# Optimization experiments

Measured on AMD Instinct MI355X. Metric: run time of the kernel, lower is better.

## Reference

```python
import jax, jax.numpy as jnp
import numpy as np

NP_, NB_, E_, BE_ = 10000, 30000, 300000, 8192
PIN, BIN, EA = 128, 128, 16
HID, GH = 64, 4
D, TH, L, NC, SEQ = 128, 4, 2, 10, 6


def _ln(x, g, b, eps=1e-5):
    m = x.mean(-1, keepdims=True)
    v = ((x - m) ** 2).mean(-1, keepdims=True)
    return (x - m) * jax.lax.rsqrt(v + eps) * g + b


def _seg_softmax(e, seg, n):
    m = jax.ops.segment_max(e, seg, num_segments=n)
    m = jnp.where(jnp.isfinite(m), m, 0.0)
    ex = jnp.exp(e - m[seg])
    s = jax.ops.segment_sum(ex, seg, num_segments=n)
    return ex / (s[seg] + 1e-16)


def _gatv2(xs, xd, es, ed, ea, Wl, bl, Wr, br, We, att, bias, n_dst):
    # PyG GATv2Conv, concat=False, add_self_loops=False, eval mode (no dropout)
    xl = (xs @ Wl + bl).reshape(-1, GH, HID)   # [Ns,H,C] source transform (message content)
    xr = (xd @ Wr + br).reshape(-1, GH, HID)   # [Nd,H,C] dest transform
    eh = (ea @ We).reshape(-1, GH, HID)        # [E,H,C] edge transform (no bias in PyG)
    msg = xl[es] + xr[ed] + eh                 # [E,H,C]
    score = jnp.einsum('ehc,hc->eh', jax.nn.leaky_relu(msg, 0.2), att)
    alpha = _seg_softmax(score, ed, n_dst)     # softmax over in-edges per dest node
    out = jax.ops.segment_sum(alpha[..., None] * xl[es], ed, num_segments=n_dst)
    return out.mean(axis=1) + bias             # concat=False -> mean over heads


def _mha(x, Wqkv, bqkv, Wo, bo):
    S, d = x.shape
    dh = d // TH
    q, k, v = jnp.split(x @ Wqkv + bqkv, 3, axis=-1)
    q = q.reshape(S, TH, dh).transpose(1, 0, 2)
    k = k.reshape(S, TH, dh).transpose(1, 0, 2)
    v = v.reshape(S, TH, dh).transpose(1, 0, 2)
    a = jax.nn.softmax(jnp.einsum('hqd,hkd->hqk', q, k) / jnp.sqrt(jnp.float32(dh)), axis=-1)
    o = jnp.einsum('hqk,hkd->hqd', a, v).transpose(1, 0, 2).reshape(S, d)
    return o @ Wo + bo


def _forward(pitcher_feat, batter_feat, edge_attr, history_states,
             Wp, bp, Wb, bb,
             rel_Wl, rel_bl, rel_Wr, rel_br, rel_We, rel_att, rel_bias,
             rev_Wl, rev_bl, rev_Wr, rev_br, rev_We, rev_att, rev_bias,
             Wgs, bgs, Wet, bet, pos,
             Wqkv, bqkv, Wo, bo, ln1g, ln1b, W1, b1, W2, b2, ln2g, ln2b,
             Wc1, bc1, Wc2, bc2,
             edge_src, edge_dst, edge_ids):
    gelu = lambda t: jax.nn.gelu(t, approximate=False)
    px = gelu(pitcher_feat @ Wp + bp)
    bx = gelu(batter_feat @ Wb + bb)
    # ('pitcher','faces','batter'): messages pitcher->batter, aggregated at batter nodes
    h_b = gelu(_gatv2(px, bx, edge_src, edge_dst, edge_attr,
                      rel_Wl, rel_bl, rel_Wr, rel_br, rel_We, rel_att, rel_bias, bx.shape[0]))
    # reversed relation: batter->pitcher, aggregated at pitcher nodes
    h_p = gelu(_gatv2(bx, px, edge_dst, edge_src, edge_attr,
                      rev_Wl, rev_bl, rev_Wr, rev_br, rev_We, rev_att, rev_bias, px.shape[0]))
    state = jnp.concatenate([h_p.mean(0), h_b.mean(0), edge_attr.mean(0)], -1) @ Wgs + bgs
    tok = jnp.concatenate([h_p[edge_src[edge_ids]], h_b[edge_dst[edge_ids]],
                           edge_attr[edge_ids]], -1) @ Wet + bet
    x = jnp.concatenate([history_states, state[None]], 0) + pos[:SEQ]
    for i in range(L):  # post-LN TransformerEncoderLayer, gelu activation, eval (no dropout)
        x = _ln(x + _mha(x, Wqkv[i], bqkv[i], Wo[i], bo[i]), ln1g[i], ln1b[i])
        f = gelu(x @ W1[i] + b1[i]) @ W2[i] + b2[i]
        x = _ln(x + f, ln2g[i], ln2b[i])
    ctx = x[-1]
    cat = jnp.concatenate([tok, jnp.broadcast_to(ctx, (tok.shape[0], D))], -1)
    return gelu(cat @ Wc1 + bc1) @ Wc2 + bc2


def setup_inputs() -> dict:
    key = jax.random.key(0)
    ks = iter(jax.random.split(key, 64))
    nrm = lambda shape, s: jax.random.normal(next(ks), shape, dtype=jnp.float32) * s
    d = {
        'pitcher_feat': nrm((NP_, PIN), 1.0),
        'batter_feat': nrm((NB_, BIN), 1.0),
        'edge_attr': nrm((E_, EA), 1.0),
        'history_states': nrm((SEQ - 1, D), 1.0),
        'Wp': nrm((PIN, HID), 0.05), 'bp': jnp.zeros((HID,), jnp.float32),
        'Wb': nrm((BIN, HID), 0.05), 'bb': jnp.zeros((HID,), jnp.float32),
    }
    for p in ('rel', 'rev'):
        d[p + '_Wl'] = nrm((HID, GH * HID), 0.05)
        d[p + '_bl'] = jnp.zeros((GH * HID,), jnp.float32)
        d[p + '_Wr'] = nrm((HID, GH * HID), 0.05)
        d[p + '_br'] = jnp.zeros((GH * HID,), jnp.float32)
        d[p + '_We'] = nrm((EA, GH * HID), 0.05)
        d[p + '_att'] = nrm((GH, HID), 0.05)
        d[p + '_bias'] = jnp.zeros((HID,), jnp.float32)
    cin = 2 * HID + EA
    d['Wgs'] = nrm((cin, D), 0.05); d['bgs'] = jnp.zeros((D,), jnp.float32)
    d['Wet'] = nrm((cin, D), 0.05); d['bet'] = jnp.zeros((D,), jnp.float32)
    d['pos'] = nrm((SEQ, D), 0.02)
    d['Wqkv'] = nrm((L, D, 3 * D), 0.05); d['bqkv'] = jnp.zeros((L, 3 * D), jnp.float32)
    d['Wo'] = nrm((L, D, D), 0.05); d['bo'] = jnp.zeros((L, D), jnp.float32)
    d['ln1g'] = jnp.ones((L, D), jnp.float32); d['ln1b'] = jnp.zeros((L, D), jnp.float32)
    d['W1'] = nrm((L, D, 4 * D), 0.05); d['b1'] = jnp.zeros((L, 4 * D), jnp.float32)
    d['W2'] = nrm((L, 4 * D, D), 0.05); d['b2'] = jnp.zeros((L, D), jnp.float32)
    d['ln2g'] = jnp.ones((L, D), jnp.float32); d['ln2b'] = jnp.zeros((L, D), jnp.float32)
    d['Wc1'] = nrm((2 * D, D), 0.05); d['bc1'] = jnp.zeros((D,), jnp.float32)
    d['Wc2'] = nrm((D, NC), 0.05); d['bc2'] = jnp.zeros((NC,), jnp.float32)
    d['edge_src'] = jax.random.randint(next(ks), (E_,), 0, NP_)
    d['edge_dst'] = jax.random.randint(next(ks), (E_,), 0, NB_)
    d['edge_ids'] = jax.random.randint(next(ks), (BE_,), 0, E_)
    return d


def reference(pitcher_feat, batter_feat, edge_attr, history_states,
              Wp, bp, Wb, bb,
              rel_Wl, rel_bl, rel_Wr, rel_br, rel_We, rel_att, rel_bias,
              rev_Wl, rev_bl, rev_Wr, rev_br, rev_We, rev_att, rev_bias,
              Wgs, bgs, Wet, bet, pos,
              Wqkv, bqkv, Wo, bo, ln1g, ln1b, W1, b1, W2, b2, ln2g, ln2b,
              Wc1, bc1, Wc2, bc2,
              edge_src, edge_dst, edge_ids):
    return _forward(pitcher_feat, batter_feat, edge_attr, history_states,
                    Wp, bp, Wb, bb,
                    rel_Wl, rel_bl, rel_Wr, rel_br, rel_We, rel_att, rel_bias,
                    rev_Wl, rev_bl, rev_Wr, rev_br, rev_We, rev_att, rev_bias,
                    Wgs, bgs, Wet, bet, pos,
                    Wqkv, bqkv, Wo, bo, ln1g, ln1b, W1, b1, W2, b2, ln2g, ln2b,
                    Wc1, bc1, Wc2, bc2,
                    edge_src, edge_dst, edge_ids)
```

## Files before the change

kernel.cpp:

```cpp
#include <hip/hip_runtime.h>
#include <math.h>

#define NP 10000
#define NB 30000
#define NEDGE 300000
#define BEDGE 8192
#define EAD 16
#define HID 64
#define GH 4
#define CW 256
#define DD 128
#define SEQ 6
#define NCLS 10
#define L 2

__device__ __forceinline__ float geluf(float x){
  return 0.5f * x * (1.0f + erff(x * 0.7071067811865475f));
}

__device__ __forceinline__ float b2f(unsigned short u){
  unsigned v = ((unsigned)u) << 16;
  return __int_as_float(v);
}
__device__ __forceinline__ unsigned short f2b(float f){
  unsigned x = __float_as_uint(f);
  unsigned r = x + 0x7FFF + ((x >> 16) & 1);
  return (unsigned short)(r >> 16);
}

typedef __attribute__((ext_vector_type(8))) short bf16x8;
typedef __attribute__((ext_vector_type(4))) float f32x4;

template<int KQ, int NTILES, bool A_F32, bool GELU>
__device__ __forceinline__
void mfma_gemm_body(int bid, const void* __restrict__ Av, const float* __restrict__ W,
                    const float* __restrict__ bias, unsigned short* __restrict__ out,
                    int M, unsigned short* __restrict__ sWt)
{
  constexpr int N  = NTILES * 16;
  constexpr int KP = KQ + 8;
  int t = threadIdx.x, w = t >> 6, l = t & 63;
  int c = l & 15, g = l >> 4;
  for (int idx = t; idx < KQ*N; idx += 256){
    int k = idx / N, n = idx - k*N;
    sWt[n*KP + k] = f2b(W[idx]);
  }
  __syncthreads();
  int rowbase = bid*64 + w*16;
  int arow = rowbase + c; if (arow > M-1) arow = M-1;
  f32x4 acc[NTILES] = {};
  #pragma unroll
  for (int ks = 0; ks < KQ/32; ++ks){
    int koff = ks*32 + g*8;
    bf16x8 a;
    if constexpr (A_F32){
      const float* Af = (const float*)Av + (size_t)arow*KQ + koff;
      float4 f0 = *(const float4*)Af;
      float4 f1 = *(const float4*)(Af + 4);
      a[0]=(short)f2b(f0.x); a[1]=(short)f2b(f0.y); a[2]=(short)f2b(f0.z); a[3]=(short)f2b(f0.w);
      a[4]=(short)f2b(f1.x); a[5]=(short)f2b(f1.y); a[6]=(short)f2b(f1.z); a[7]=(short)f2b(f1.w);
    } else {
      a = *(const bf16x8*)((const unsigned short*)Av + (size_t)arow*KQ + koff);
    }
    #pragma unroll
    for (int nt = 0; nt < NTILES; ++nt){
      bf16x8 b = *(const bf16x8*)&sWt[(nt*16 + c)*KP + koff];
      acc[nt] = __builtin_amdgcn_mfma_f32_16x16x32_bf16(a, b, acc[nt], 0, 0, 0);
    }
  }
  #pragma unroll
  for (int nt = 0; nt < NTILES; ++nt){
    #pragma unroll
    for (int j = 0; j < 4; ++j){
      int row = rowbase + g*4 + j;
      if (row < M){
        int col = nt*16 + c;
        float v = acc[nt][j] + bias[col];
        if (GELU) v = geluf(v);
        out[(size_t)row*N + col] = f2b(v);
      }
    }
  }
}

__global__ __launch_bounds__(256)
void k1_count_enc(const int* __restrict__ edst, const int* __restrict__ esrc,
                  int* __restrict__ degA, int* __restrict__ degB,
                  const float* __restrict__ pit, const float* __restrict__ Wp,
                  const float* __restrict__ bp, unsigned short* __restrict__ px,
                  const float* __restrict__ bat, const float* __restrict__ Wb,
                  const float* __restrict__ bb, unsigned short* __restrict__ bx,
                  int nbCount, int nbP)
{
  __shared__ unsigned short sWt[64*136];
  int b = blockIdx.x;
  if (b < nbCount){
    int i = b*256 + threadIdx.x;
// ... 15 lines not shown
  int t = threadIdx.x, w = t >> 6, l = t & 63;
  if (t == 0) sbase = 0;
  __syncthreads();
  for (int base = 0; base < n; base += 4096){
    int i = base + t*4;
    int4 v = make_int4(0,0,0,0);
    if (i < n) v = *(const int4*)(deg + i);
    int tsum = v.x + v.y + v.z + v.w;
    int x = tsum;
    #pragma unroll
    for (int off = 1; off < 64; off <<= 1){
      int y = __shfl_up(x, off);
      if (l >= off) x += y;
    }
    if (l == 63) wsum[w] = x;
    __syncthreads();
    int woff = 0, tot = 0;
    #pragma unroll
    for (int ww = 0; ww < 16; ++ww){
      int wv = wsum[ww];
      if (ww < w) woff += wv;
      tot += wv;
    }
    int excl = sbase + woff + x - tsum;
    if (i < n){
      int e1 = excl + v.x, e2 = excl + v.x + v.y, e3 = excl + v.x + v.y + v.z;
      row_start[i]   = excl; cursor[i]   = excl;
      row_start[i+1] = e1;   cursor[i+1] = e1;
      row_start[i+2] = e2;   cursor[i+2] = e2;
      row_start[i+3] = e3;   cursor[i+3] = e3;
    }
    __syncthreads();
    if (t == 0) sbase += tot;
    __syncthreads();
  }
  if (t == 0) row_start[n] = sbase;
}

__global__ __launch_bounds__(1024)
void scan2_kernel(const int* __restrict__ degA, int* __restrict__ rsA, int* __restrict__ curA, int nA,
                  const int* __restrict__ degB, int* __restrict__ rsB, int* __restrict__ curB, int nB,
                  float* __restrict__ mvec){
  if (blockIdx.x == 0){
    scan_dev(degA, rsA, curA, nA);
  } else {
    if (threadIdx.x < 144) mvec[threadIdx.x] = 0.f;
    scan_dev(degB, rsB, curB, nB);
  }
}

__global__ __launch_bounds__(256)
void k2_scatter_proj(const int* __restrict__ edst, const int* __restrict__ esrc,
                     int* __restrict__ curA, int* __restrict__ curB,
                     int2* __restrict__ csrA, int2* __restrict__ csrB,
                     const unsigned short* __restrict__ px, const unsigned short* __restrict__ bx,
                     const float* __restrict__ rel_Wl, const float* __restrict__ rel_bl,
                     const float* __restrict__ rel_Wr, const float* __restrict__ rel_br,
                     const float* __restrict__ rev_Wl, const float* __restrict__ rev_bl,
                     const float* __restrict__ rev_Wr, const float* __restrict__ rev_br,
                     unsigned short* __restrict__ xlA, unsigned short* __restrict__ xrA,
                     unsigned short* __restrict__ xlB, unsigned short* __restrict__ xrB,
                     int nbScat, int nbP, int nbB)
{
  __shared__ unsigned short sWt[256*72];
  int b = blockIdx.x;
  if (b < nbScat){
    int i = b*256 + threadIdx.x;
    if (i < NEDGE){
      int d = edst[i], s = esrc[i];
      int p = atomicAdd(&curA[d], 1);
      csrA[p] = make_int2(i, s);
      int q = atomicAdd(&curB[s], 1);
      csrB[q] = make_int2(i, d);
    }
  } else {
    b -= nbScat;
    if (b < nbP)               mfma_gemm_body<64,16,false,false>(b,            px, rel_Wl, rel_bl, xlA, NP, sWt);
    else if (b < nbP + nbB)    mfma_gemm_body<64,16,false,false>(b-nbP,        bx, rel_Wr, rel_br, xrA, NB, sWt);
    else if (b < nbP + 2*nbB)  mfma_gemm_body<64,16,false,false>(b-nbP-nbB,    bx, rev_Wl, rev_bl, xlB, NB, sWt);
    else                       mfma_gemm_body<64,16,false,false>(b-nbP-2*nbB,  px, rev_Wr, rev_br, xrB, NP, sWt);
  }
}

#define GAT_PAIR(X0, X1, EV0, EV1, V1OK, P0MASK)                             \
  {                                                                          \
    float x0 = b2f(X0.x), x1 = b2f(X0.y), x2 = b2f(X0.z), x3 = b2f(X0.w);    \
    float y0 = b2f(X1.x), y1 = b2f(X1.y), y2 = b2f(X1.z), y3 = b2f(X1.w);    \
    float h00 = x0 + r0, h01 = x1 + r1, h02 = x2 + r2, h03 = x3 + r3;        \
    float h10 = y0 + r0, h11 = y1 + r1, h12 = y2 + r2, h13 = y3 + r3;        \
    int ia0 = __float_as_int(EV0);                                           \
    int ia1 = __float_as_int(EV1);                                           \
    _Pragma("unroll")                                                        \
    for (int k = 0; k < EAD; ++k){                                           \
      float c0 = __int_as_float(__builtin_amdgcn_readlane(ia0, k));          \
      float c1 = __int_as_float(__builtin_amdgcn_readlane(ia1, k));          \
      float4 wv = *(const float4*)&sWe[k*CW + 4*l];                          \
      h00 = fmaf(c0, wv.x, h00); h01 = fmaf(c0, wv.y, h01);                  \
      h02 = fmaf(c0, wv.z, h02); h03 = fmaf(c0, wv.w, h03);                  \
      h10 = fmaf(c1, wv.x, h10); h11 = fmaf(c1, wv.y, h11);                  \
      h12 = fmaf(c1, wv.z, h12); h13 = fmaf(c1, wv.w, h13);                  \
    }                                                                        \
    h00 = (h00 > 0.f ? h00 : 0.2f*h00) * at.x;                               \
    h01 = (h01 > 0.f ? h01 : 0.2f*h01) * at.y;                               \
    h02 = (h02 > 0.f ? h02 : 0.2f*h02) * at.z;                               \
    h03 = (h03 > 0.f ? h03 : 0.2f*h03) * at.w;                               \
    h10 = (h10 > 0.f ? h10 : 0.2f*h10) * at.x;                               \
    h11 = (h11 > 0.f ? h11 : 0.2f*h11) * at.y;                               \
    h12 = (h12 > 0.f ? h12 : 0.2f*h12) * at.z;                               \
    h13 = (h13 > 0.f ? h13 : 0.2f*h13) * at.w;                               \
    float g0 = (h00 + h01) + (h02 + h03);                                    \
    float g1 = (h10 + h11) + (h12 + h13);                                    \
    _Pragma("unroll")                                                        \
    for (int off = 1; off < 16; off <<= 1){                                  \
      g0 += __shfl_xor(g0, off);                                             \
      g1 += __shfl_xor(g1, off);                                             \
    }                                                                        \
    float gm = (V1OK) ? fmaxf(g0, g1) : g0;                                  \
    float mn = fmaxf(m, gm);                                                 \
    float cc = __expf(m - mn);                                               \
    float p0 = __expf(g0 - mn);                                              \
    if (!(P0MASK)) p0 = 0.f;                                                 \
    float p1 = (V1OK) ? __expf(g1 - mn) : 0.f;                               \
    s  = fmaf(s, cc, p0 + p1);                                               \
    a0 = fmaf(a0, cc, fmaf(p1, y0, p0*x0));                                  \
    a1 = fmaf(a1, cc, fmaf(p1, y1, p0*x1));                                  \
    a2 = fmaf(a2, cc, fmaf(p1, y2, p0*x2));                                  \
    a3 = fmaf(a3, cc, fmaf(p1, y3, p0*x3));                                  \
    m = mn;                                                                  \
  }

__global__ __launch_bounds__(256)
void gat2_kernel(const unsigned short* __restrict__ xlA_, const unsigned short* __restrict__ xrA_,
                 const float* __restrict__ WeA, const float* __restrict__ attA,
                 const float* __restrict__ biasA, const int2* __restrict__ csrA_,
                 const int* __restrict__ rsA_, float* __restrict__ houtA,
                 const unsigned short* __restrict__ xlB_, const unsigned short* __restrict__ xrB_,
                 const float* __restrict__ WeB, const float* __restrict__ attB,
                 const float* __restrict__ biasB, const int2* __restrict__ csrB_,
                 const int* __restrict__ rsB_, float* __restrict__ houtB,
                 const float* __restrict__ ea, int gsplit)
{
  __shared__ float sWe[16*CW];
  bool isA = (int)blockIdx.x < gsplit;
  const unsigned short* xl = isA ? xlA_ : xlB_;
  const unsigned short* xr = isA ? xrA_ : xrB_;
  const float* We   = isA ? WeA   : WeB;
  const float* att  = isA ? attA  : attB;
  const float* bias = isA ? biasA : biasB;
  const int2* csr   = isA ? csrA_ : csrB_;
  const int* row_start = isA ? rsA_ : rsB_;
  float* hout = isA ? houtA : houtB;
  int ndst = isA ? NB : NP;
  int bid  = isA ? (int)blockIdx.x : (int)blockIdx.x - gsplit;
  int nblk = isA ? gsplit : (int)gridDim.x - gsplit;

  int t = threadIdx.x, l = t & 63;
  for (int i = t*4; i < 16*CW; i += 1024)
    *(float4*)&sWe[i] = *(const float4*)&We[i];
  __syncthreads();
  float4 at = *(const float4*)&att[4*l];
  float4 bi = *(const float4*)&bias[(l & 15)*4];
  int wid = bid*4 + (t >> 6);
  int nw = nblk*4;
  for (int d = wid; d < ndst; d += nw){
    ushort4 ru = *(const ushort4*)(xr + (size_t)d*CW + 4*l);
    float r0 = b2f(ru.x), r1 = b2f(ru.y), r2 = b2f(ru.z), r3 = b2f(ru.w);
    int rs = row_start[d], re = row_start[d+1];
    float m = -INFINITY, s = 0.f;
    float a0 = 0.f, a1 = 0.f, a2 = 0.f, a3 = 0.f;
    if (rs < re){
      int last = re - 1;
      #define CLMP(x) ((x) > last ? last : (x))
      int2 qA0 = csr[rs],         qA1 = csr[CLMP(rs+1)];
      int2 qB0 = csr[CLMP(rs+2)], qB1 = csr[CLMP(rs+3)];
      int2 nA0 = csr[CLMP(rs+4)], nA1 = csr[CLMP(rs+5)];
      int2 nB0 = csr[CLMP(rs+6)], nB1 = csr[CLMP(rs+7)];
      ushort4 xA0 = *(const ushort4*)(xl + (size_t)qA0.y*CW + 4*l);
      ushort4 xA1 = *(const ushort4*)(xl + (size_t)qA1.y*CW + 4*l);
      float  evA0 = ea[(size_t)qA0.x*EAD + (l & 15)];
      float  evA1 = ea[(size_t)qA1.x*EAD + (l & 15)];
      ushort4 xB0 = *(const ushort4*)(xl + (size_t)qB0.y*CW + 4*l);
      ushort4 xB1 = *(const ushort4*)(xl + (size_t)qB1.y*CW + 4*l);
      float  evB0 = ea[(size_t)qB0.x*EAD + (l & 15)];
      float  evB1 = ea[(size_t)qB1.x*EAD + (l & 15)];
      for (int i = rs; i < re; i += 4){
        int2 mA0 = csr[CLMP(i+8)],  mA1 = csr[CLMP(i+9)];
        int2 mB0 = csr[CLMP(i+10)], mB1 = csr[CLMP(i+11)];
        GAT_PAIR(xA0, xA1, evA0, evA1, (i+1 < re), true);
        xA0 = *(const ushort4*)(xl + (size_t)nA0.y*CW + 4*l);
        xA1 = *(const ushort4*)(xl + (size_t)nA1.y*CW + 4*l);
        evA0 = ea[(size_t)nA0.x*EAD + (l & 15)];
        evA1 = ea[(size_t)nA1.x*EAD + (l & 15)];
        nA0 = mA0; nA1 = mA1;
        GAT_PAIR(xB0, xB1, evB0, evB1, (i+3 < re), (i+2 < re));
        xB0 = *(const ushort4*)(xl + (size_t)nB0.y*CW + 4*l);
        xB1 = *(const ushort4*)(xl + (size_t)nB1.y*CW + 4*l);
        evB0 = ea[(size_t)nB0.x*EAD + (l & 15)];
        evB1 = ea[(size_t)nB1.x*EAD + (l & 15)];
        nB0 = mB0; nB1 = mB1;
      }
      #undef CLMP
    }
    float inv = 1.f / (s + 1e-16f);
    float v0 = a0*inv, v1 = a1*inv, v2 = a2*inv, v3 = a3*inv;
    v0 += __shfl_xor(v0, 16); v1 += __shfl_xor(v1, 16);
    v2 += __shfl_xor(v2, 16); v3 += __shfl_xor(v3, 16);
    v0 += __shfl_xor(v0, 32); v1 += __shfl_xor(v1, 32);
    v2 += __shfl_xor(v2, 32); v3 += __shfl_xor(v3, 32);
    if (l < 16){
      float4 o;
      o.x = geluf(v0*0.25f + bi.x);
      o.y = geluf(v1*0.25f + bi.y);
      o.z = geluf(v2*0.25f + bi.z);
      o.w = geluf(v3*0.25f + bi.w);
      *(float4*)(hout + (size_t)d*HID + 4*l) = o;
    }
  }
}

__device__ __forceinline__ void colsum_seg(int bid, int nb, const float4* __restrict__ in4,
                                           long total4, int n4, float* __restrict__ out,
                                           float scale, float* lds){
  int t = threadIdx.x, l = t & 63, w = t >> 6;
  long gid = (long)bid*256 + t;
  long stride = (long)nb*256;
  float4 acc = make_float4(0.f,0.f,0.f,0.f);
  for (long i = gid; i < total4; i += stride){
    float4 v = in4[i];
    acc.x += v.x; acc.y += v.y; acc.z += v.z; acc.w += v.w;
  }
  for (int off = n4; off < 64; off <<= 1){
    acc.x += __shfl_xor(acc.x, off);
    acc.y += __shfl_xor(acc.y, off);
    acc.z += __shfl_xor(acc.z, off);
    acc.w += __shfl_xor(acc.w, off);
  }
  if (l < n4) *(float4*)&lds[(w*n4 + l)*4] = acc;
  __syncthreads();
  if (t < n4*4){
    float sum = lds[t] + lds[n4*4 + t] + lds[2*n4*4 + t] + lds[3*n4*4 + t];
    atomicAdd(&out[t], sum * scale);
  }
  __syncthreads();
}

__device__ void colsum3_body(int bid, int nb, const float* __restrict__ hp,
                             const float* __restrict__ hb, const float* __restrict__ ea,
                             float* __restrict__ mvec){
  __shared__ float lds[4*16*4];
  colsum_seg(bid, nb, (const float4*)ea, (long)NEDGE*EAD/4, 4,  mvec+128, 1.f/NEDGE, lds);
  colsum_seg(bid, nb, (const float4*)hb, (long)NB*HID/4,    16, mvec+64,  1.f/NB,    lds);
  colsum_seg(bid, nb, (const float4*)hp, (long)NP*HID/4,    16, mvec,     1.f/NP,    lds);
}

__device__ void gemmcat_body(int bid, const float* __restrict__ hp, const float* __restrict__ hb,
                             const float* __restrict__ ea, const int* __restrict__ esrc,
                             const int* __restrict__ edst, const int* __restrict__ eids,
                             const float* __restrict__ W, const float* __restrict__ bias,
                             float* __restrict__ out)
{
  __shared__ float sAT[16][68];
  __shared__ float sB[16][68];
  __shared__ int sS[64], sD[64], sE[64];
  int t = threadIdx.x;
  int m0 = (bid >> 1)*64, n0 = (bid & 1)*64;
  if (t < 64){
    int e = eids[m0 + t];
    sS[t] = esrc[e]; sD[t] = edst[e]; sE[t] = e;
  }
  __syncthreads();
  int tr = t >> 4, tc = t & 15;
  float acc[4][4] = {};
  for (int k0 = 0; k0 < 144; k0 += 16){
    {
      int r = t >> 2, c = (t & 3) * 4;
      const float* src; int col = k0 + c;
      if (k0 < 64)       { src = hp + (size_t)sS[r]*HID; }
      else if (k0 < 128) { src = hb + (size_t)sD[r]*HID; col -= 64; }
      else               { src = ea + (size_t)sE[r]*EAD; col -= 128; }
      float4 va = *(const float4*)(src + col);
      sAT[c+0][r] = va.x; sAT[c+1][r] = va.y; sAT[c+2][r] = va.z; sAT[c+3][r] = va.w;
    }
    {
      int r = t >> 4, c = (t & 15) * 4;
      float4 vb = *(const float4*)(W + (size_t)(k0+r)*DD + n0 + c);
      *(float4*)&sB[r][c] = vb;
    }
    __syncthreads();
    #pragma unroll
    for (int k = 0; k < 16; ++k){
      float4 av = *(const float4*)&sAT[k][tr*4];
      float4 bv = *(const float4*)&sB[k][tc*4];
      acc[0][0] = fmaf(av.x, bv.x, acc[0][0]);
      acc[0][1] = fmaf(av.x, bv.y, acc[0][1]);
      acc[0][2] = fmaf(av.x, bv.z, acc[0][2]);
      acc[0][3] = fmaf(av.x, bv.w, acc[0][3]);
      acc[1][0] = fmaf(av.y, bv.x, acc[1][0]);
      acc[1][1] = fmaf(av.y, bv.y, acc[1][1]);
      acc[1][2] = fmaf(av.y, bv.z, acc[1][2]);
      acc[1][3] = fmaf(av.y, bv.w, acc[1][3]);
      acc[2][0] = fmaf(av.z, bv.x, acc[2][0]);
      acc[2][1] = fmaf(av.z, bv.y, acc[2][1]);
      acc[2][2] = fmaf(av.z, bv.z, acc[2][2]);
      acc[2][3] = fmaf(av.z, bv.w, acc[2][3]);
      acc[3][0] = fmaf(av.w, bv.x, acc[3][0]);
      acc[3][1] = fmaf(av.w, bv.y, acc[3][1]);
      acc[3][2] = fmaf(av.w, bv.z, acc[3][2]);
      acc[3][3] = fmaf(av.w, bv.w, acc[3][3]);
    }
    __syncthreads();
  }
  #pragma unroll
  for (int i = 0; i < 4; ++i){
    int gr = m0 + tr*4 + i;
    float4 v;
    v.x = acc[i][0] + bias[n0 + tc*4 + 0];
    v.y = acc[i][1] + bias[n0 + tc*4 + 1];
    v.z = acc[i][2] + bias[n0 + tc*4 + 2];
    v.w = acc[i][3] + bias[n0 + tc*4 + 3];
    *(float4*)(out + (size_t)gr*DD + n0 + tc*4) = v;
  }
}

__global__ __launch_bounds__(256)
void k3_colsum_gemmcat(const float* __restrict__ hp, const float* __restrict__ hb,
                       const float* __restrict__ ea, float* __restrict__ mvec,
                       const int* __restrict__ esrc, const int* __restrict__ edst,
                       const int* __restrict__ eids, const float* __restrict__ Wet,
                       const float* __restrict__ bet, float* __restrict__ tokb,
                       int nbCol)
{
  int b = blockIdx.x;
  if (b < nbCol) colsum3_body(b, nbCol, hp, hb, ea, mvec);
  else           gemmcat_body(b - nbCol, hp, hb, ea, esrc, edst, eids, Wet, bet, tokb);
}

template<int K, int N, int NC>
__device__ __forceinline__ void qstageF(const float* __restrict__ x,
                                        const float* __restrict__ W,
                                        float (&a)[6][4], int q, int ch)
{
  constexpr int NQ = N/4;
  constexpr int KC = K/NC;
  constexpr int J  = KC/4;
  const float4* wp = (const float4*)W + (size_t)(ch*KC)*NQ + q;
  const float* xb = x + ch*KC;
  float4 wv[KC];
  int kx[J];
  #pragma unroll
  for (int j = 0; j < J; ++j){
    int k4 = (j + ch) & (J-1);
    kx[j] = k4;
    wv[j*4+0] = wp[(size_t)(k4*4+0)*NQ];
    wv[j*4+1] = wp[(size_t)(k4*4+1)*NQ];
    wv[j*4+2] = wp[(size_t)(k4*4+2)*NQ];
    wv[j*4+3] = wp[(size_t)(k4*4+3)*NQ];
  }
  #pragma unroll
  for (int s = 0; s < 6; ++s){ a[s][0]=0.f; a[s][1]=0.f; a[s][2]=0.f; a[s][3]=0.f; }
  #pragma unroll
  for (int j = 0; j < J; ++j){
    #pragma unroll
    for (int s = 0; s < 6; ++s){
      float4 xv = *(const float4*)&xb[s*K + kx[j]*4];
      a[s][0]=fmaf(xv.x,wv[j*4+0].x,a[s][0]); a[s][0]=fmaf(xv.y,wv[j*4+1].x,a[s][0]);
      a[s][0]=fmaf(xv.z,wv[j*4+2].x,a[s][0]); a[s][0]=fmaf(xv.w,wv[j*4+3].x,a[s][0]);
      a[s][1]=fmaf(xv.x,wv[j*4+0].y,a[s][1]); a[s][1]=fmaf(xv.y,wv[j*4+1].y,a[s][1]);
      a[s][1]=fmaf(xv.z,wv[j*4+2].y,a[s][1]); a[s][1]=fmaf(xv.w,wv[j*4+3].y,a[s][1]);
      a[s][2]=fmaf(xv.x,wv[j*4+0].z,a[s][2]); a[s][2]=fmaf(xv.y,wv[j*4+1].z,a[s][2]);
      a[s][2]=fmaf(xv.z,wv[j*4+2].z,a[s][2]); a[s][2]=fmaf(xv.w,wv[j*4+3].z,a[s][2]);
      a[s][3]=fmaf(xv.x,wv[j*4+0].w,a[s][3]); a[s][3]=fmaf(xv.y,wv[j*4+1].w,a[s][3]);
      a[s][3]=fmaf(xv.z,wv[j*4+2].w,a[s][3]); a[s][3]=fmaf(xv.w,wv[j*4+3].w,a[s][3]);
    }
  }
  #pragma unroll
  for (int off = 1; off < NC; off <<= 1){
    #pragma unroll
    for (int s = 0; s < 6; ++s){
      a[s][0]+=__shfl_xor(a[s][0],off); a[s][1]+=__shfl_xor(a[s][1],off);
      a[s][2]+=__shfl_xor(a[s][2],off); a[s][3]+=__shfl_xor(a[s][3],off);
    }
  }
}

__global__ __launch_bounds__(512)
void xform_kernel(const float* __restrict__ hist, const float* __restrict__ mvec,
                  const float* __restrict__ Wgs, const float* __restrict__ bgs,
                  const float* __restrict__ pos,
                  const float* __restrict__ Wqkv, const float* __restrict__ bqkv,
                  const float* __restrict__ Wo, const float* __restrict__ bo,
                  const float* __restrict__ ln1g, const float* __restrict__ ln1b,
                  const float* __restrict__ W1, const float* __restrict__ b1,
                  const float* __restrict__ W2, const float* __restrict__ b2,
                  const float* __restrict__ ln2g, const float* __restrict__ ln2b,
                  const float* __restrict__ Wc1, const float* __restrict__ bc1,
                  float* __restrict__ bias2)
{
  __shared__ float sx[SEQ*DD];
  __shared__ float sq[SEQ*3*DD];
  __shared__ float sh[SEQ*512];
  __shared__ float st[SEQ*DD];
  __shared__ float sc[4][6][6];
  __shared__ float smv[144];
  int t = threadIdx.x;

  for (int i = t; i < (SEQ-1)*DD; i += 512) sx[i] = hist[i] + pos[i];
  if (t < 144) smv[t] = mvec[t];
  __syncthreads();
  if (t < 256){
    int q = t >> 3, ch = t & 7;
    float4 wv[18];
    #pragma unroll
    for (int kk = 0; kk < 18; ++kk)
      wv[kk] = *(const float4*)&Wgs[(ch*18+kk)*DD + q*4];
    float a0=0.f,a1=0.f,a2=0.f,a3=0.f;
    #pragma unroll
    for (int kk = 0; kk < 18; ++kk){
// ... 122 lines not shown
    }
    __syncthreads();
    {
      int q = t >> 4, ch = t & 15;
      const float* w2 = W2 + (size_t)lyr*512*DD;
      const float* b2p = b2 + lyr*DD;
      float a[6][4];
      qstageF<512,128,16>(sh, w2, a, q, ch);
      if (ch == 0){
        int n = q*4;
        #pragma unroll
        for (int s = 0; s < 6; ++s){
          st[s*128+n+0]=a[s][0]+b2p[n+0]+sx[s*128+n+0];
          st[s*128+n+1]=a[s][1]+b2p[n+1]+sx[s*128+n+1];
          st[s*128+n+2]=a[s][2]+b2p[n+2]+sx[s*128+n+2];
          st[s*128+n+3]=a[s][3]+b2p[n+3]+sx[s*128+n+3];
        }
      }
    }
    __syncthreads();
    {
      int w = t >> 6, lw = t & 63;
      if (w < SEQ){
        const float* g = ln2g + lyr*DD; const float* be = ln2b + lyr*DD;
        float v0 = st[w*DD + lw], v1 = st[w*DD + 64 + lw];
        float sm = v0 + v1;
        #pragma unroll
        for (int off = 1; off < 64; off <<= 1) sm += __shfl_xor(sm, off);
        float mean = sm * 0.0078125f;
        float d0 = v0-mean, d1 = v1-mean;
        float qv = d0*d0 + d1*d1;
        #pragma unroll
        for (int off = 1; off < 64; off <<= 1) qv += __shfl_xor(qv, off);
        float inv = rsqrtf(qv*0.0078125f + 1e-5f);
        sx[w*DD + lw]      = d0*inv*g[lw] + be[lw];
        sx[w*DD + 64 + lw] = d1*inv*g[64+lw] + be[64+lw];
      }
    }
    __syncthreads();
  }
  if (t < 256){
    int q = t >> 3, ch = t & 7;
    const float4* wp = (const float4*)(Wc1 + (size_t)DD*DD) + (size_t)(ch*16)*32 + q;
    const float* xb = &sx[(SEQ-1)*DD + ch*16];
    float4 wv[16];
    int kx[4];
    #pragma unroll
    for (int j = 0; j < 4; ++j){
      int k4 = (j + ch) & 3;
      kx[j] = k4;
      wv[j*4+0] = wp[(size_t)(k4*4+0)*32];
      wv[j*4+1] = wp[(size_t)(k4*4+1)*32];
      wv[j*4+2] = wp[(size_t)(k4*4+2)*32];
      wv[j*4+3] = wp[(size_t)(k4*4+3)*32];
    }
    float a0=0.f,a1=0.f,a2=0.f,a3=0.f;
    #pragma unroll
    for (int j = 0; j < 4; ++j){
      float4 xv = *(const float4*)&xb[kx[j]*4];
      a0=fmaf(xv.x,wv[j*4+0].x,a0); a0=fmaf(xv.y,wv[j*4+1].x,a0);
      a0=fmaf(xv.z,wv[j*4+2].x,a0); a0=fmaf(xv.w,wv[j*4+3].x,a0);
      a1=fmaf(xv.x,wv[j*4+0].y,a1); a1=fmaf(xv.y,wv[j*4+1].y,a1);
      a1=fmaf(xv.z,wv[j*4+2].y,a1); a1=fmaf(xv.w,wv[j*4+3].y,a1);
      a2=fmaf(xv.x,wv[j*4+0].z,a2); a2=fmaf(xv.y,wv[j*4+1].z,a2);
      a2=fmaf(xv.z,wv[j*4+2].z,a2); a2=fmaf(xv.w,wv[j*4+3].z,a2);
      a3=fmaf(xv.x,wv[j*4+0].w,a3); a3=fmaf(xv.y,wv[j*4+1].w,a3);
      a3=fmaf(xv.z,wv[j*4+2].w,a3); a3=fmaf(xv.w,wv[j*4+3].w,a3);
    }
    #pragma unroll
    for (int off = 1; off < 8; off <<= 1){
      a0+=__shfl_xor(a0,off); a1+=__shfl_xor(a1,off);
      a2+=__shfl_xor(a2,off); a3+=__shfl_xor(a3,off);
    }
    if (ch == 0){
      int n = q*4;
      bias2[n+0]=a0+bc1[n+0];
      bias2[n+1]=a1+bc1[n+1];
      bias2[n+2]=a2+bc1[n+2];
      bias2[n+3]=a3+bc1[n+3];
    }
  }
}

template<bool GELU>
__global__ __launch_bounds__(256)
void gemm64_kernel(const float* __restrict__ A, const float* __restrict__ W,
                   const float* __restrict__ bias, float* __restrict__ out,
                   int M, int K, int N)
{
  __shared__ float sAT[16][68];
  __shared__ float sB[16][68];
  int t = threadIdx.x;
  int m0 = blockIdx.x * 64, n0 = blockIdx.y * 64;
  int tr = t >> 4, tc = t & 15;
  float acc[4][4] = {};
  for (int k0 = 0; k0 < K; k0 += 16){
    {
      int r = t >> 2, c = (t & 3) * 4;
      int gr = m0 + r;
      float4 va = make_float4(0.f,0.f,0.f,0.f);
      if (gr < M) va = *(const float4*)(A + (size_t)gr*K + k0 + c);
      sAT[c+0][r] = va.x; sAT[c+1][r] = va.y; sAT[c+2][r] = va.z; sAT[c+3][r] = va.w;
    }
    {
      int r = t >> 4, c = (t & 15) * 4;
      float4 vb = *(const float4*)(W + (size_t)(k0+r)*N + n0 + c);
      *(float4*)&sB[r][c] = vb;
    }
    __syncthreads();
    #pragma unroll
    for (int k = 0; k < 16; ++k){
      float4 av = *(const float4*)&sAT[k][tr*4];
      float4 bv = *(const float4*)&sB[k][tc*4];
      acc[0][0] = fmaf(av.x, bv.x, acc[0][0]);
      acc[0][1] = fmaf(av.x, bv.y, acc[0][1]);
      acc[0][2] = fmaf(av.x, bv.z, acc[0][2]);
      acc[0][3] = fmaf(av.x, bv.w, acc[0][3]);
      acc[1][0] = fmaf(av.y, bv.x, acc[1][0]);
      acc[1][1] = fmaf(av.y, bv.y, acc[1][1]);
      acc[1][2] = fmaf(av.y, bv.z, acc[1][2]);
      acc[1][3] = fmaf(av.y, bv.w, acc[1][3]);
      acc[2][0] = fmaf(av.z, bv.x, acc[2][0]);
      acc[2][1] = fmaf(av.z, bv.y, acc[2][1]);
      acc[2][2] = fmaf(av.z, bv.z, acc[2][2]);
      acc[2][3] = fmaf(av.z, bv.w, acc[2][3]);
      acc[3][0] = fmaf(av.w, bv.x, acc[3][0]);
      acc[3][1] = fmaf(av.w, bv.y, acc[3][1]);
      acc[3][2] = fmaf(av.w, bv.z, acc[3][2]);
      acc[3][3] = fmaf(av.w, bv.w, acc[3][3]);
    }
    __syncthreads();
  }
  #pragma unroll
  for (int i = 0; i < 4; ++i){
    int gr = m0 + tr*4 + i;
    if (gr < M){
      float4 v;
      v.x = acc[i][0] + bias[n0 + tc*4 + 0];
      v.y = acc[i][1] + bias[n0 + tc*4 + 1];
      v.z = acc[i][2] + bias[n0 + tc*4 + 2];
      v.w = acc[i][3] + bias[n0 + tc*4 + 3];
      if (GELU){ v.x = geluf(v.x); v.y = geluf(v.y); v.z = geluf(v.z); v.w = geluf(v.w); }
      *(float4*)(out + (size_t)gr*N + n0 + tc*4) = v;
    }
  }
}

__global__ void head2_kernel(const float* __restrict__ hid, const float* __restrict__ Wc2,
                             const float* __restrict__ bc2, float* __restrict__ out){
  int i = blockIdx.x*blockDim.x + threadIdx.x;
  if (i >= BEDGE*16) return;
  int tok = i >> 4, c = i & 15;
  if (c < NCLS){
    float acc = bc2[c];
    const float4* hr4 = (const float4*)(hid + (size_t)tok*DD);
    #pragma unroll 8
    for (int k4 = 0; k4 < 32; ++k4){
      float4 hv = hr4[k4];
      acc = fmaf(hv.x, Wc2[(4*k4+0)*NCLS + c], acc);
      acc = fmaf(hv.y, Wc2[(4*k4+1)*NCLS + c], acc);
      acc = fmaf(hv.z, Wc2[(4*k4+2)*NCLS + c], acc);
      acc = fmaf(hv.w, Wc2[(4*k4+3)*NCLS + c], acc);
    }
    out[tok*NCLS + c] = acc;
  }
}

extern "C" void kernel_launch(void* const* d_in, const int* in_sizes, int n_in,
                              void* d_out, int out_size, void* d_ws, size_t ws_size,
                              hipStream_t stream){
  (void)in_sizes; (void)n_in; (void)out_size; (void)ws_size;
  const float* pitcher = (const float*)d_in[0];
  const float* batter  = (const float*)d_in[1];
  const float* eattr   = (const float*)d_in[2];
  const float* hist    = (const float*)d_in[3];
  const float* Wp = (const float*)d_in[4];
  const float* bp = (const float*)d_in[5];
  const float* Wb = (const float*)d_in[6];
  const float* bb = (const float*)d_in[7];
  const float* rel_Wl  = (const float*)d_in[8];
  const float* rel_bl  = (const float*)d_in[9];
  const float* rel_Wr  = (const float*)d_in[10];
  const float* rel_br  = (const float*)d_in[11];
  const float* rel_We  = (const float*)d_in[12];
  const float* rel_att = (const float*)d_in[13];
  const float* rel_bias= (const float*)d_in[14];
  const float* rev_Wl  = (const float*)d_in[15];
  const float* rev_bl  = (const float*)d_in[16];
  const float* rev_Wr  = (const float*)d_in[17];
  const float* rev_br  = (const float*)d_in[18];
  const float* rev_We  = (const float*)d_in[19];
  const float* rev_att = (const float*)d_in[20];
  const float* rev_bias= (const float*)d_in[21];
  const float* Wgs = (const float*)d_in[22];
  const float* bgs = (const float*)d_in[23];
  const float* Wet = (const float*)d_in[24];
  const float* bet = (const float*)d_in[25];
  const float* pos = (const float*)d_in[26];
  const float* Wqkv= (const float*)d_in[27];
  const float* bqkv= (const float*)d_in[28];
  const float* Wo  = (const float*)d_in[29];
  const float* bo  = (const float*)d_in[30];
  const float* ln1g= (const float*)d_in[31];
  const float* ln1b= (const float*)d_in[32];
  const float* W1  = (const float*)d_in[33];
  const float* b1  = (const float*)d_in[34];
  const float* W2  = (const float*)d_in[35];
  const float* b2  = (const float*)d_in[36];
  const float* ln2g= (const float*)d_in[37];
  const float* ln2b= (const float*)d_in[38];
  const float* Wc1 = (const float*)d_in[39];
  const float* bc1 = (const float*)d_in[40];
  const float* Wc2 = (const float*)d_in[41];
  const float* bc2 = (const float*)d_in[42];
  const int* esrc = (const int*)d_in[43];
  const int* edst = (const int*)d_in[44];
  const int* eids = (const int*)d_in[45];

  char* w = (char*)d_ws;
  size_t off = 0;
  auto alloc = [&](size_t bytes)->void*{
    void* p = (void*)(w + off);
    off += (bytes + 255) & ~(size_t)255;
    return p;
  };
  unsigned short* px_bf  = (unsigned short*)alloc((size_t)NP*HID*2);
  unsigned short* bx_bf  = (unsigned short*)alloc((size_t)NB*HID*2);
  float*          hp     = (float*)alloc((size_t)NP*HID*4);
  float*          hb     = (float*)alloc((size_t)NB*HID*4);
  unsigned short* xlA    = (unsigned short*)alloc((size_t)NP*CW*2);
  unsigned short* xrA    = (unsigned short*)alloc((size_t)NB*CW*2);
  unsigned short* xlB    = (unsigned short*)alloc((size_t)NB*CW*2);
  unsigned short* xrB    = (unsigned short*)alloc((size_t)NP*CW*2);
  int*            degAB  = (int*)alloc((size_t)(NB+NP)*4);
  int*            degA   = degAB;
  int*            degB   = degAB + NB;
  int*            rowstA = (int*)alloc((size_t)(NB+1)*4);
  int*            rowstB = (int*)alloc((size_t)(NP+1)*4);
  int*            cursA  = (int*)alloc((size_t)NB*4);
  int*            cursB  = (int*)alloc((size_t)NP*4);
  int2*           csrA   = (int2*)alloc((size_t)NEDGE*8);
  int2*           csrB   = (int2*)alloc((size_t)NEDGE*8);
  float*          mvec   = (float*)alloc(144*4);
  float*          bias2  = (float*)alloc(DD*4);
  float*          tokb   = (float*)xlA;
  float*          hid    = (float*)xrA;

  const int nbCount = (NEDGE + 255)/256;
  const int nbP = (NP + 63)/64;
  const int nbB = (NB + 63)/64;

  hipMemsetAsync(degAB, 0, (size_t)(NB+NP)*4, stream);
  k1_count_enc<<<nbCount + nbP + nbB, 256, 0, stream>>>(
      edst, esrc, degA, degB,
      pitcher, Wp, bp, px_bf, batter, Wb, bb, bx_bf, nbCount, nbP);

  scan2_kernel<<<2, 1024, 0, stream>>>(degA, rowstA, cursA, NB,
                                       degB, rowstB, cursB, NP, mvec);

  k2_scatter_proj<<<nbCount + 2*nbP + 2*nbB, 256, 0, stream>>>(
      edst, esrc, cursA, cursB, csrA, csrB, px_bf, bx_bf,
      rel_Wl, rel_bl, rel_Wr, rel_br, rev_Wl, rev_bl, rev_Wr, rev_br,
      xlA, xrA, xlB, xrB, nbCount, nbP, nbB);

  gat2_kernel<<<4096, 256, 0, stream>>>(
      xlA, xrA, rel_We, rel_att, rel_bias, csrA, rowstA, hb,
      xlB, xrB, rev_We, rev_att, rev_bias, csrB, rowstB, hp,
      eattr, 2048);

  k3_colsum_gemmcat<<<512, 256, 0, stream>>>(
      hp, hb, eattr, mvec, esrc, edst, eids, Wet, bet, tokb, 256);

  xform_kernel<<<1, 512, 0, stream>>>(
      hist, mvec, Wgs, bgs, pos, Wqkv, bqkv, Wo, bo, ln1g, ln1b,
      W1, b1, W2, b2, ln2g, ln2b, Wc1, bc1, bias2);

  gemm64_kernel<true><<<dim3(BEDGE/64,2), 256, 0, stream>>>(tokb, Wc1, bias2, hid, BEDGE, DD, DD);
  head2_kernel<<<(BEDGE*16+255)/256, 256, 0, stream>>>(hid, Wc2, bc2, (float*)d_out);
}
```

Baseline: 387.3 us.

## Fuse column means into GAT epilogue and merge classifier GEMM with head

The column-mean reduction of hp and hb now happens inside the GAT kernel's epilogue, with per-warp sums combined through shared memory and atomics. The edge-attr column sum runs in 64 extra blocks of the same launch, so hp and hb no longer have to be re-read afterwards. The GAT inner loop keeps the edge weight matrix in registers instead of shared memory. It also drops the running-max online softmax for a plain exp-sum, which removes the rescaling work but can overflow if attention scores are large. The Wc1 GEMM plus GELU and the 10-class head are fused into one kernel that stages the hidden tile in LDS, which removes an intermediate global buffer and a launch.

```diff
diff --git a/kernel.cpp b/kernel.cpp
--- a/kernel.cpp
+++ b/kernel.cpp
@@ -13,6 +13,7 @@
 #define SEQ 6
 #define NCLS 10
 #define L 2
+#define NEACOL 64
 
 __device__ __forceinline__ float geluf(float x){
   return 0.5f * x * (1.0f + erff(x * 0.7071067811865475f));
@@ -194,6 +195,32 @@
   }
 }
 
+__device__ __forceinline__ void colsum_seg(int bid, int nb, const float4* __restrict__ in4,
+                                           long total4, int n4, float* __restrict__ out,
+                                           float scale, float* lds){
+  int t = threadIdx.x, l = t & 63, w = t >> 6;
+  long gid = (long)bid*256 + t;
+  long stride = (long)nb*256;
+  float4 acc = make_float4(0.f,0.f,0.f,0.f);
+  for (long i = gid; i < total4; i += stride){
+    float4 v = in4[i];
+    acc.x += v.x; acc.y += v.y; acc.z += v.z; acc.w += v.w;
+  }
+  for (int off = n4; off < 64; off <<= 1){
+    acc.x += __shfl_xor(acc.x, off);
+    acc.y += __shfl_xor(acc.y, off);
+    acc.z += __shfl_xor(acc.z, off);
+    acc.w += __shfl_xor(acc.w, off);
+  }
+  if (l < n4) *(float4*)&lds[(w*n4 + l)*4] = acc;
+  __syncthreads();
+  if (t < n4*4){
+    float sum = lds[t] + lds[n4*4 + t] + lds[2*n4*4 + t] + lds[3*n4*4 + t];
+    atomicAdd(&out[t], sum * scale);
+  }
+  __syncthreads();
+}
+
 #define GAT_PAIR(X0, X1, EV0, EV1, V1OK, P0MASK)                             \
   {                                                                          \
     float x0 = b2f(X0.x), x1 = b2f(X0.y), x2 = b2f(X0.z), x3 = b2f(X0.w);    \
@@ -206,20 +233,19 @@
     for (int k = 0; k < EAD; ++k){                                           \
       float c0 = __int_as_float(__builtin_amdgcn_readlane(ia0, k));          \
       float c1 = __int_as_float(__builtin_amdgcn_readlane(ia1, k));          \
-      float4 wv = *(const float4*)&sWe[k*CW + 4*l];                          \
-      h00 = fmaf(c0, wv.x, h00); h01 = fmaf(c0, wv.y, h01);                  \
-      h02 = fmaf(c0, wv.z, h02); h03 = fmaf(c0, wv.w, h03);                  \
-      h10 = fmaf(c1, wv.x, h10); h11 = fmaf(c1, wv.y, h11);                  \
-      h12 = fmaf(c1, wv.z, h12); h13 = fmaf(c1, wv.w, h13);                  \
+      h00 = fmaf(c0, wv[k].x, h00); h01 = fmaf(c0, wv[k].y, h01);            \
+      h02 = fmaf(c0, wv[k].z, h02); h03 = fmaf(c0, wv[k].w, h03);            \
+      h10 = fmaf(c1, wv[k].x, h10); h11 = fmaf(c1, wv[k].y, h11);            \
+      h12 = fmaf(c1, wv[k].z, h12); h13 = fmaf(c1, wv[k].w, h13);            \
     }                                                                        \
-    h00 = (h00 > 0.f ? h00 : 0.2f*h00) * at.x;                               \
-    h01 = (h01 > 0.f ? h01 : 0.2f*h01) * at.y;                               \
-    h02 = (h02 > 0.f ? h02 : 0.2f*h02) * at.z;                               \
-    h03 = (h03 > 0.f ? h03 : 0.2f*h03) * at.w;                               \
-    h10 = (h10 > 0.f ? h10 : 0.2f*h10) * at.x;                               \
-    h11 = (h11 > 0.f ? h11 : 0.2f*h11) * at.y;                               \
-    h12 = (h12 > 0.f ? h12 : 0.2f*h12) * at.z;                               \
-    h13 = (h13 > 0.f ? h13 : 0.2f*h13) * at.w;                               \
+    h00 = fmaxf(h00, 0.2f*h00) * at.x;                                       \
+    h01 = fmaxf(h01, 0.2f*h01) * at.y;                                       \
+    h02 = fmaxf(h02, 0.2f*h02) * at.z;                                       \
+    h03 = fmaxf(h03, 0.2f*h03) * at.w;                                       \
+    h10 = fmaxf(h10, 0.2f*h10) * at.x;                                       \
+    h11 = fmaxf(h11, 0.2f*h11) * at.y;                                       \
+    h12 = fmaxf(h12, 0.2f*h12) * at.z;                                       \
+    h13 = fmaxf(h13, 0.2f*h13) * at.w;                                       \
     float g0 = (h00 + h01) + (h02 + h03);                                    \
     float g1 = (h10 + h11) + (h12 + h13);                                    \
     _Pragma("unroll")                                                        \
@@ -227,18 +253,13 @@
       g0 += __shfl_xor(g0, off);                                             \
       g1 += __shfl_xor(g1, off);                                             \
     }                                                                        \
-    float gm = (V1OK) ? fmaxf(g0, g1) : g0;                                  \
-    float mn = fmaxf(m, gm);                                                 \
-    float cc = __expf(m - mn);                                               \
-    float p0 = __expf(g0 - mn);                                              \
-    if (!(P0MASK)) p0 = 0.f;                                                 \
-    float p1 = (V1OK) ? __expf(g1 - mn) : 0.f;                               \
-    s  = fmaf(s, cc, p0 + p1);                                               \
-    a0 = fmaf(a0, cc, fmaf(p1, y0, p0*x0));                                  \
-    a1 = fmaf(a1, cc, fmaf(p1, y1, p0*x1));                                  \
-    a2 = fmaf(a2, cc, fmaf(p1, y2, p0*x2));                                  \
-    a3 = fmaf(a3, cc, fmaf(p1, y3, p0*x3));                                  \
-    m = mn;                                                                  \
+    float p0 = (P0MASK) ? __expf(g0) : 0.f;                                  \
+    float p1 = (V1OK) ? __expf(g1) : 0.f;                                    \
+    s += p0 + p1;                                                            \
+    a0 = fmaf(p0, x0, fmaf(p1, y0, a0));                                     \
+    a1 = fmaf(p0, x1, fmaf(p1, y1, a1));                                     \
+    a2 = fmaf(p0, x2, fmaf(p1, y2, a2));                                     \
+    a3 = fmaf(p0, x3, fmaf(p1, y3, a3));                                     \
   }
 
 __global__ __launch_bounds__(256)
@@ -250,10 +271,19 @@
                  const float* __restrict__ WeB, const float* __restrict__ attB,
                  const float* __restrict__ biasB, const int2* __restrict__ csrB_,
                  const int* __restrict__ rsB_, float* __restrict__ houtB,
-                 const float* __restrict__ ea, int gsplit)
+                 const float* __restrict__ ea, float* __restrict__ mvec, int gsplit)
 {
-  __shared__ float sWe[16*CW];
-  bool isA = (int)blockIdx.x < gsplit;
+  __shared__ float csum[4][16][4];
+  int t = threadIdx.x, l = t & 63;
+  int b = blockIdx.x;
+  if (b < NEACOL){
+    colsum_seg(b, NEACOL, (const float4*)ea, (long)NEDGE*EAD/4, 4,
+               mvec + 128, 1.f/NEDGE, &csum[0][0][0]);
+    return;
+  }
+  b -= NEACOL;
+  int ngat = (int)gridDim.x - NEACOL;
+  bool isA = b < gsplit;
   const unsigned short* xl = isA ? xlA_ : xlB_;
   const unsigned short* xr = isA ? xrA_ : xrB_;
   const float* We   = isA ? WeA   : WeB;
@@ -263,22 +293,23 @@
   const int* row_start = isA ? rsA_ : rsB_;
   float* hout = isA ? houtA : houtB;
   int ndst = isA ? NB : NP;
-  int bid  = isA ? (int)blockIdx.x : (int)blockIdx.x - gsplit;
-  int nblk = isA ? gsplit : (int)gridDim.x - gsplit;
-
-  int t = threadIdx.x, l = t & 63;
-  for (int i = t*4; i < 16*CW; i += 1024)
-    *(float4*)&sWe[i] = *(const float4*)&We[i];
-  __syncthreads();
+  int bid  = isA ? b : b - gsplit;
+  int nblk = isA ? gsplit : ngat - gsplit;
+
+  float4 wv[EAD];
+  #pragma unroll
+  for (int k = 0; k < EAD; ++k)
+    wv[k] = *(const float4*)&We[k*CW + 4*l];
   float4 at = *(const float4*)&att[4*l];
   float4 bi = *(const float4*)&bias[(l & 15)*4];
+  float cs0 = 0.f, cs1 = 0.f, cs2 = 0.f, cs3 = 0.f;
   int wid = bid*4 + (t >> 6);
   int nw = nblk*4;
   for (int d = wid; d < ndst; d += nw){
     ushort4 ru = *(const ushort4*)(xr + (size_t)d*CW + 4*l);
     float r0 = b2f(ru.x), r1 = b2f(ru.y), r2 = b2f(ru.z), r3 = b2f(ru.w);
     int rs = row_start[d], re = row_start[d+1];
-    float m = -INFINITY, s = 0.f;
+    float s = 0.f;
     float a0 = 0.f, a1 = 0.f, a2 = 0.f, a3 = 0.f;
     if (rs < re){
       int last = re - 1;
@@ -326,43 +357,22 @@
       o.z = geluf(v2*0.25f + bi.z);
       o.w = geluf(v3*0.25f + bi.w);
       *(float4*)(hout + (size_t)d*HID + 4*l) = o;
-    }
-  }
-}
-
-__device__ __forceinline__ void colsum_seg(int bid, int nb, const float4* __restrict__ in4,
-                                           long total4, int n4, float* __restrict__ out,
-                                           float scale, float* lds){
-  int t = threadIdx.x, l = t & 63, w = t >> 6;
-  long gid = (long)bid*256 + t;
-  long stride = (long)nb*256;
-  float4 acc = make_float4(0.f,0.f,0.f,0.f);
-  for (long i = gid; i < total4; i += stride){
-    float4 v = in4[i];
-    acc.x += v.x; acc.y += v.y; acc.z += v.z; acc.w += v.w;
-  }
-  for (int off = n4; off < 64; off <<= 1){
-    acc.x += __shfl_xor(acc.x, off);
-    acc.y += __shfl_xor(acc.y, off);
-    acc.z += __shfl_xor(acc.z, off);
-    acc.w += __shfl_xor(acc.w, off);
-  }
-  if (l < n4) *(float4*)&lds[(w*n4 + l)*4] = acc;
+      cs0 += o.x; cs1 += o.y; cs2 += o.z; cs3 += o.w;
+    }
+  }
+  int w = t >> 6;
+  if (l < 16){
+    csum[w][l][0] = cs0; csum[w][l][1] = cs1;
+    csum[w][l][2] = cs2; csum[w][l][3] = cs3;
+  }
   __syncthreads();
-  if (t < n4*4){
-    float sum = lds[t] + lds[n4*4 + t] + lds[2*n4*4 + t] + lds[3*n4*4 + t];
-    atomicAdd(&out[t], sum * scale);
-  }
-  __syncthreads();
-}
-
-__device__ void colsum3_body(int bid, int nb, const float* __restrict__ hp,
-                             const float* __restrict__ hb, const float* __restrict__ ea,
-                             float* __restrict__ mvec){
-  __shared__ float lds[4*16*4];
-  colsum_seg(bid, nb, (const float4*)ea, (long)NEDGE*EAD/4, 4,  mvec+128, 1.f/NEDGE, lds);
-  colsum_seg(bid, nb, (const float4*)hb, (long)NB*HID/4,    16, mvec+64,  1.f/NB,    lds);
-  colsum_seg(bid, nb, (const float4*)hp, (long)NP*HID/4,    16, mvec,     1.f/NP,    lds);
+  if (t < 64){
+    int lq = t >> 2, j = t & 3;
+    float sum = csum[0][lq][j] + csum[1][lq][j] + csum[2][lq][j] + csum[3][lq][j];
+    float scale = isA ? (1.f/NB) : (1.f/NP);
+    float* dst = isA ? (mvec + 64) : mvec;
+    atomicAdd(&dst[t], sum * scale);
+  }
 }
 
 __device__ void gemmcat_body(int bid, const float* __restrict__ hp, const float* __restrict__ hb,
@@ -435,16 +445,13 @@
 }
 
 __global__ __launch_bounds__(256)
-void k3_colsum_gemmcat(const float* __restrict__ hp, const float* __restrict__ hb,
-                       const float* __restrict__ ea, float* __restrict__ mvec,
-                       const int* __restrict__ esrc, const int* __restrict__ edst,
-                       const int* __restrict__ eids, const float* __restrict__ Wet,
-                       const float* __restrict__ bet, float* __restrict__ tokb,
-                       int nbCol)
+void gemmcat_kernel(const float* __restrict__ hp, const float* __restrict__ hb,
+                    const float* __restrict__ ea, const int* __restrict__ esrc,
+                    const int* __restrict__ edst, const int* __restrict__ eids,
+                    const float* __restrict__ Wet, const float* __restrict__ bet,
+                    float* __restrict__ tokb)
 {
-  int b = blockIdx.x;
-  if (b < nbCol) colsum3_body(b, nbCol, hp, hb, ea, mvec);
-  else           gemmcat_body(b - nbCol, hp, hb, ea, esrc, edst, eids, Wet, bet, tokb);
+  gemmcat_body(blockIdx.x, hp, hb, ea, esrc, edst, eids, Wet, bet, tokb);
 }
 
 template<int K, int N, int NC>
@@ -733,87 +740,73 @@
   }
 }
 
-template<bool GELU>
 __global__ __launch_bounds__(256)
-void gemm64_kernel(const float* __restrict__ A, const float* __restrict__ W,
-                   const float* __restrict__ bias, float* __restrict__ out,
-                   int M, int K, int N)
+void cls_kernel(const float* __restrict__ A, const float* __restrict__ W,
+                const float* __restrict__ bias2, const float* __restrict__ Wc2,
+                const float* __restrict__ bc2, float* __restrict__ out)
 {
   __shared__ float sAT[16][68];
-  __shared__ float sB[16][68];
+  __shared__ float sB[16][132];
+  __shared__ float sH[64][129];
   int t = threadIdx.x;
-  int m0 = blockIdx.x * 64, n0 = blockIdx.y * 64;
+  int m0 = blockIdx.x * 64;
   int tr = t >> 4, tc = t & 15;
-  float acc[4][4] = {};
-  for (int k0 = 0; k0 < K; k0 += 16){
+  float acc[4][8] = {};
+  for (int k0 = 0; k0 < DD; k0 += 16){
     {
       int r = t >> 2, c = (t & 3) * 4;
-      int gr = m0 + r;
-      float4 va = make_float4(0.f,0.f,0.f,0.f);
-      if (gr < M) va = *(const float4*)(A + (size_t)gr*K + k0 + c);
+      float4 va = *(const float4*)(A + (size_t)(m0+r)*DD + k0 + c);
       sAT[c+0][r] = va.x; sAT[c+1][r] = va.y; sAT[c+2][r] = va.z; sAT[c+3][r] = va.w;
     }
     {
-      int r = t >> 4, c = (t & 15) * 4;
-      float4 vb = *(const float4*)(W + (size_t)(k0+r)*N + n0 + c);
-      *(float4*)&sB[r][c] = vb;
+      int r = t >> 4, c = (t & 15) * 8;
+      float4 b0 = *(const float4*)(W + (size_t)(k0+r)*DD + c);
+      float4 b1 = *(const float4*)(W + (size_t)(k0+r)*DD + c + 4);
+      *(float4*)&sB[r][c] = b0;
+      *(float4*)&sB[r][c+4] = b1;
     }
     __syncthreads();
     #pragma unroll
     for (int k = 0; k < 16; ++k){
       float4 av = *(const float4*)&sAT[k][tr*4];
-      float4 bv = *(const float4*)&sB[k][tc*4];
-      acc[0][0] = fmaf(av.x, bv.x, acc[0][0]);
-      acc[0][1] = fmaf(av.x, bv.y, acc[0][1]);
-      acc[0][2] = fmaf(av.x, bv.z, acc[0][2]);
-      acc[0][3] = fmaf(av.x, bv.w, acc[0][3]);
-      acc[1][0] = fmaf(av.y, bv.x, acc[1][0]);
-      acc[1][1] = fmaf(av.y, bv.y, acc[1][1]);
-      acc[1][2] = fmaf(av.y, bv.z, acc[1][2]);
-      acc[1][3] = fmaf(av.y, bv.w, acc[1][3]);
-      acc[2][0] = fmaf(av.z, bv.x, acc[2][0]);
-      acc[2][1] = fmaf(av.z, bv.y, acc[2][1]);
-      acc[2][2] = fmaf(av.z, bv.z, acc[2][2]);
-      acc[2][3] = fmaf(av.z, bv.w, acc[2][3]);
-      acc[3][0] = fmaf(av.w, bv.x, acc[3][0]);
-      acc[3][1] = fmaf(av.w, bv.y, acc[3][1]);
-      acc[3][2] = fmaf(av.w, bv.z, acc[3][2]);
-      acc[3][3] = fmaf(av.w, bv.w, acc[3][3]);
+      float4 b0 = *(const float4*)&sB[k][tc*8];
+      float4 b1 = *(const float4*)&sB[k][tc*8+4];
+      #pragma unroll
+      for (int i = 0; i < 4; ++i){
+        float avi = (i==0)?av.x:(i==1)?av.y:(i==2)?av.z:av.w;
+        acc[i][0] = fmaf(avi, b0.x, acc[i][0]);
+        acc[i][1] = fmaf(avi, b0.y, acc[i][1]);
+        acc[i][2] = fmaf(avi, b0.z, acc[i][2]);
+        acc[i][3] = fmaf(avi, b0.w, acc[i][3]);
+        acc[i][4] = fmaf(avi, b1.x, acc[i][4]);
+        acc[i][5] = fmaf(avi, b1.y, acc[i][5]);
+        acc[i][6] = fmaf(avi, b1.z, acc[i][6]);
+        acc[i][7] = fmaf(avi, b1.w, acc[i][7]);
+      }
     }
     __syncthreads();
   }
   #pragma unroll
   for (int i = 0; i < 4; ++i){
-    int gr = m0 + tr*4 + i;
-    if (gr < M){
-      float4 v;
-      v.x = acc[i][0] + bias[n0 + tc*4 + 0];
-      v.y = acc[i][1] + bias[n0 + tc*4 + 1];
-      v.z = acc[i][2] + bias[n0 + tc*4 + 2];
-      v.w = acc[i][3] + bias[n0 + tc*4 + 3];
-      if (GELU){ v.x = geluf(v.x); v.y = geluf(v.y); v.z = geluf(v.z); v.w = geluf(v.w); }
-      *(float4*)(out + (size_t)gr*N + n0 + tc*4) = v;
-    }
-  }
-}
-
-__global__ void head2_kernel(const float* __restrict__ hid, const float* __restrict__ Wc2,
-                             const float* __restrict__ bc2, float* __restrict__ out){
-  int i = blockIdx.x*blockDim.x + threadIdx.x;
-  if (i >= BEDGE*16) return;
-  int tok = i >> 4, c = i & 15;
-  if (c < NCLS){
-    float acc = bc2[c];
-    const float4* hr4 = (const float4*)(hid + (size_t)tok*DD);
-    #pragma unroll 8
-    for (int k4 = 0; k4 < 32; ++k4){
-      float4 hv = hr4[k4];
-      acc = fmaf(hv.x, Wc2[(4*k4+0)*NCLS + c], acc);
-      acc = fmaf(hv.y, Wc2[(4*k4+1)*NCLS + c], acc);
-      acc = fmaf(hv.z, Wc2[(4*k4+2)*NCLS + c], acc);
-      acc = fmaf(hv.w, Wc2[(4*k4+3)*NCLS + c], acc);
-    }
-    out[tok*NCLS + c] = acc;
+    #pragma unroll
+    for (int j = 0; j < 8; ++j){
+      sH[tr*4+i][tc*8+j] = geluf(acc[i][j] + bias2[tc*8+j]);
+    }
+  }
+  __syncthreads();
+  if (t < 64){
+    float a10[NCLS];
+    #pragma unroll
+    for (int c = 0; c < NCLS; ++c) a10[c] = bc2[c];
+    for (int k = 0; k < DD; ++k){
+      float hv = sH[t][k];
+      #pragma unroll
+      for (int c = 0; c < NCLS; ++c)
+        a10[c] = fmaf(hv, Wc2[k*NCLS + c], a10[c]);
+    }
+    #pragma unroll
+    for (int c = 0; c < NCLS; ++c)
+      out[(size_t)(m0+t)*NCLS + c] = a10[c];
   }
 }
 
@@ -895,7 +888,6 @@
   float*          mvec   = (float*)alloc(144*4);
   float*          bias2  = (float*)alloc(DD*4);
   float*          tokb   = (float*)xlA;
-  float*          hid    = (float*)xrA;
 
   const int nbCount = (NEDGE + 255)/256;
   const int nbP = (NP + 63)/64;
@@ -914,18 +906,17 @@
       rel_Wl, rel_bl, rel_Wr, rel_br, rev_Wl, rev_bl, rev_Wr, rev_br,
       xlA, xrA, xlB, xrB, nbCount, nbP, nbB);
 
-  gat2_kernel<<<4096, 256, 0, stream>>>(
+  gat2_kernel<<<NEACOL + 4096, 256, 0, stream>>>(
       xlA, xrA, rel_We, rel_att, rel_bias, csrA, rowstA, hb,
       xlB, xrB, rev_We, rev_att, rev_bias, csrB, rowstB, hp,
-      eattr, 2048);
-
-  k3_colsum_gemmcat<<<512, 256, 0, stream>>>(
-      hp, hb, eattr, mvec, esrc, edst, eids, Wet, bet, tokb, 256);
+      eattr, mvec, 2048);
+
+  gemmcat_kernel<<<256, 256, 0, stream>>>(
+      hp, hb, eattr, esrc, edst, eids, Wet, bet, tokb);
 
   xform_kernel<<<1, 512, 0, stream>>>(
       hist, mvec, Wgs, bgs, pos, Wqkv, bqkv, Wo, bo, ln1g, ln1b,
       W1, b1, W2, b2, ln2g, ln2b, Wc1, bc1, bias2);
 
-  gemm64_kernel<true><<<dim3(BEDGE/64,2), 256, 0, stream>>>(tokb, Wc1, bias2, hid, BEDGE, DD, DD);
-  head2_kernel<<<(BEDGE*16+255)/256, 256, 0, stream>>>(hid, Wc2, bc2, (float*)d_out);
-}
+  cls_kernel<<<BEDGE/64, 256, 0, stream>>>(tokb, Wc1, bias2, Wc2, bc2, (float*)d_out);
+}
```

Result: slower. 420.4 us (+8.5%).
